# Kernel tuning notes

Hardware: AMD Instinct MI355X
Metric: run time of the kernel (lower is better)

The kernel has to match this reference:

```python
import jax, jax.numpy as jnp
import numpy as np

LAGS = 2
SLOPE = 0.01  # nn.LeakyReLU default negative_slope


def setup_inputs() -> dict:
    key = jax.random.key(0)
    k0, k1, k2, k3, k4 = jax.random.split(key, 5)
    B, T, D, H = 64, 514, 32, 128
    IN = LAGS * D + 1
    x = jax.random.normal(k0, (B, T, D), dtype=jnp.float32)
    # per-latent-dim 2-layer MLP params (num_layers=3, layer_norm=False collapses to 2 Linears)
    W1 = jax.random.normal(k1, (D, H, IN), dtype=jnp.float32) / np.sqrt(IN).astype(np.float32)
    b1 = jax.random.normal(k2, (D, H), dtype=jnp.float32) * 0.01
    W2 = jax.random.normal(k3, (D, H), dtype=jnp.float32) / np.sqrt(H).astype(np.float32)
    b2 = jax.random.normal(k4, (D,), dtype=jnp.float32) * 0.01
    return {"x": x, "W1": W1, "b1": b1, "W2": W2, "b2": b2}


def reference(x, W1, b1, W2, b2):
    L = LAGS
    B, T, D = x.shape
    # unfold(dim=1, size=L+1, step=1) + swapaxes -> windows [B, T-L, L+1, D]
    idx = jnp.arange(T - L)[:, None] + jnp.arange(L + 1)[None, :]
    w = x[:, idx]                       # [B, T-L, L+1, D]
    w = w.reshape(-1, L + 1, D)         # [N, L+1, D]
    yy = w[:, -1, :]                    # [N, D]  current step, per dim
    xx = w[:, :-1, :].reshape(-1, L * D)  # [N, L*D] lagged history (shared)
    # batched tiny-MLP forward: input to g_i is [xx, yy[:, i]]
    pre = (jnp.einsum('nk,dhk->ndh', xx, W1[:, :, :-1])
           + yy[:, :, None] * W1[:, :, -1][None]
           + b1[None])                  # [N, D, H]
    act = jnp.where(pre >= 0, pre, SLOPE * pre)
    residuals = jnp.einsum('ndh,dh->nd', act, W2) + b2[None]  # [N, D]
    # analytic Jacobian of scalar output wrt the (L*D+1)-dim input:
    # J = (W2 * leaky'(pre)) @ W1
    dact = jnp.where(pre >= 0, jnp.float32(1.0), jnp.float32(SLOPE))
    g = dact * W2[None]                 # [N, D, H]
    jac = jnp.einsum('ndh,dhk->ndk', g, W1)  # [N, D, L*D+1]
    logabsdet = jnp.sum(jnp.log(jnp.abs(jac[:, :, -1])), axis=1)  # [N] summed over dims
    # hist_jac: torch returns a list of D tensors [N, 1, L*D]; stacked here as [D, N, 1, L*D]
    hist_jac = jnp.transpose(jac[:, :, :-1], (1, 0, 2))[:, :, None, :]
    residuals = residuals.reshape(B, T - L, D)
    sum_log_abs_det_jacobian = logabsdet.reshape(B, T - L).sum(axis=1)  # [B]
    return residuals, sum_log_abs_det_jacobian, hist_jac
```

## Files before the change

kernel.cpp:

```cpp
#include <hip/hip_runtime.h>
#include <math.h>


typedef _Float16 f16;
typedef __attribute__((ext_vector_type(8))) _Float16 half8;
typedef __attribute__((ext_vector_type(4))) _Float16 half4;
typedef __attribute__((ext_vector_type(4))) float floatx4;

namespace {
constexpr int    XS_ROW   = 40;
constexpr size_t XS_SPLIT = (size_t)64 * 514 * XS_ROW * 2;
constexpr size_t WS_XS_HI = 0;
constexpr size_t WS_XS_LO = XS_SPLIT;
constexpr int    W1_KP    = 72;
constexpr size_t W1_SPLIT = (size_t)32 * 128 * W1_KP * 2;
constexpr size_t WS_W1_HI = 2 * XS_SPLIT;
constexpr size_t WS_W1_LO = WS_W1_HI + W1_SPLIT;
constexpr int    W1T_HP   = 136;
constexpr size_t WS_W1T   = WS_W1_LO + W1_SPLIT;

constexpr int L_W1HI = 0;
constexpr int L_W1LO = 18432;
constexpr int L_GB   = 0;
constexpr int L_W1T  = 17408;
constexpr int L_XSHI = 36864;
constexpr int L_XSLO = 42144;
constexpr int L_B1   = 47424;
constexpr int L_W2   = L_B1 + 512;
constexpr int L_W64  = L_W2 + 512;
constexpr int L_YY   = L_W64 + 512;
constexpr int L_RES  = L_YY + 256;
constexpr int L_JAC  = L_RES + 1024;
constexpr int L_TOTAL = L_JAC + 1024;

constexpr size_t OUT1_OFF = (size_t)64 * 512 * 32;
constexpr size_t OUT2_OFF = OUT1_OFF + 64;
}

__global__ __launch_bounds__(256) void split_x_kernel(
    const float* __restrict__ x, f16* __restrict__ xh, f16* __restrict__ xl)
{
    int idx = blockIdx.x * 256 + threadIdx.x;
    if (idx >= 64 * 514 * 32) return;
    int row = idx >> 5, c = idx & 31;
    float v = x[idx];
    f16 hi = (f16)v;
    float r = v - (float)hi;
    xh[row * XS_ROW + c] = hi;
    xl[row * XS_ROW + c] = (f16)(r * 4096.0f);
}

__global__ __launch_bounds__(256) void split_w1_kernel(
    const float* __restrict__ W1, f16* __restrict__ wh, f16* __restrict__ wl,
    f16* __restrict__ wT)
{
    int idx = blockIdx.x * 256 + threadIdx.x;
    if (idx >= 32 * 128 * 64) return;
    int d = idx >> 13, rem = idx & 8191;
    int h = rem >> 6, k = rem & 63;
    float v = W1[((size_t)(d * 128 + h)) * 65 + k];
    f16 hi = (f16)v;
    float r = v - (float)hi;
    wh[(size_t)(d * 128 + h) * W1_KP + k] = hi;
    wl[(size_t)(d * 128 + h) * W1_KP + k] = (f16)(r * 4096.0f);
    wT[(size_t)(d * 64 + k) * W1T_HP + h] = hi;
}

__global__ __launch_bounds__(256, 3) void np_main_kernel(
    const float* __restrict__ x,
    const float* __restrict__ W1,
    const float* __restrict__ b1,
    const float* __restrict__ W2,
    const float* __restrict__ b2,
    const char* __restrict__ ws,
    float* __restrict__ out)
{
    extern __shared__ char smem[];
    const int tile = blockIdx.x;
    const int d    = blockIdx.y;
    const int b    = tile >> 3;
    const int t0   = (tile & 7) << 6;
    const int tid  = threadIdx.x;
    const int wave = tid >> 6, lane = tid & 63;
    const int c = lane & 15, q = lane >> 4;

    float* b1L  = (float*)(smem + L_B1);
    float* W2L  = (float*)(smem + L_W2);
    float* w64L = (float*)(smem + L_W64);
    float* yyL  = (float*)(smem + L_YY);
    float* resP = (float*)(smem + L_RES);
    float* jacP = (float*)(smem + L_JAC);

    {
        const float4* s1 = (const float4*)(ws + WS_W1_HI + (size_t)d * 18432);
        const float4* s2 = (const float4*)(ws + WS_W1_LO + (size_t)d * 18432);
        float4* d1 = (float4*)(smem + L_W1HI);
        float4* d2 = (float4*)(smem + L_W1LO);
        for (int i = tid; i < 1152; i += 256) { d1[i] = s1[i]; d2[i] = s2[i]; }
        const float4* s3 = (const float4*)(ws + WS_XS_HI + (size_t)(b * 514 + t0) * (XS_ROW * 2));
        const float4* s4 = (const float4*)(ws + WS_XS_LO + (size_t)(b * 514 + t0) * (XS_ROW * 2));
        float4* d3 = (float4*)(smem + L_XSHI);
        float4* d4 = (float4*)(smem + L_XSLO);
        for (int i = tid; i < 330; i += 256) { d3[i] = s3[i]; d4[i] = s4[i]; }
        if (tid < 128) {
            b1L[tid]  = b1[d * 128 + tid];
            W2L[tid]  = W2[d * 128 + tid];
            w64L[tid] = W1[(size_t)(d * 128 + tid) * 65 + 64];
        }
        if (tid < 64) yyL[tid] = x[(size_t)(b * 514 + t0 + tid + 2) * 32 + d];
    }
    __syncthreads();

    floatx4 accP[2][4], accQ[2][4];
    #pragma unroll
    for (int ht = 0; ht < 2; ++ht)
        #pragma unroll
        for (int nt = 0; nt < 4; ++nt) { accP[ht][nt] = (floatx4)0.f; accQ[ht][nt] = (floatx4)0.f; }

    #pragma unroll
    for (int ks = 0; ks < 2; ++ks) {
        half8 aH[2], aL[2], bH[4], bL[4];
        #pragma unroll
        for (int ht = 0; ht < 2; ++ht) {
            const int off = (wave * 32 + ht * 16 + c) * W1_KP + ks * 32 + q * 8;
            aH[ht] = *(const half8*)(smem + L_W1HI + off * 2);
            aL[ht] = *(const half8*)(smem + L_W1LO + off * 2);
        }
        #pragma unroll
        for (int nt = 0; nt < 4; ++nt) {
            const int off = (nt * 16 + c + ks) * XS_ROW + q * 8;
            bH[nt] = *(const half8*)(smem + L_XSHI + off * 2);
            bL[nt] = *(const half8*)(smem + L_XSLO + off * 2);
        }
        #pragma unroll
        for (int ht = 0; ht < 2; ++ht)
            #pragma unroll
            for (int nt = 0; nt < 4; ++nt) {
                accP[ht][nt] = __builtin_amdgcn_mfma_f32_16x16x32_f16(aH[ht], bH[nt], accP[ht][nt], 0, 0, 0);
                accQ[ht][nt] = __builtin_amdgcn_mfma_f32_16x16x32_f16(aH[ht], bL[nt], accQ[ht][nt], 0, 0, 0);
                accQ[ht][nt] = __builtin_amdgcn_mfma_f32_16x16x32_f16(aL[ht], bH[nt], accQ[ht][nt], 0, 0, 0);
            }
    }
    __syncthreads();

    {
        const float4* s = (const float4*)(ws + WS_W1T + (size_t)d * 17408);
        float4* dst = (float4*)(smem + L_W1T);
        for (int i = tid; i < 1088; i += 256) dst[i] = s[i];
    }
    float res[4] = {0.f, 0.f, 0.f, 0.f}, j64[4] = {0.f, 0.f, 0.f, 0.f};
    #pragma unroll
    for (int ht = 0; ht < 2; ++ht) {
        const int hbase = wave * 32 + ht * 16 + q * 4;
        #pragma unroll
        for (int nt = 0; nt < 4; ++nt) {
            const int n = nt * 16 + c;
            half4 gp;
            #pragma unroll
            for (int r = 0; r < 4; ++r) {
                const int h = hbase + r;
                const float pre = accP[ht][nt][r] + accQ[ht][nt][r] * (1.0f / 4096.0f)
                                + b1L[h] + yyL[n] * w64L[h];
                const float gg = (pre >= 0.f ? 1.0f : 0.01f) * W2L[h];
                res[nt] += pre * gg;
                j64[nt] += gg * w64L[h];
                gp[r] = (f16)gg;
            }
            *(half4*)(smem + L_GB + (n * W1T_HP + hbase) * 2) = gp;
        }
    }
    #pragma unroll
    for (int nt = 0; nt < 4; ++nt) {
        float rv = res[nt];
        rv += __shfl_xor(rv, 16, 64);
        rv += __shfl_xor(rv, 32, 64);
        float jv = j64[nt];
        jv += __shfl_xor(jv, 16, 64);
        jv += __shfl_xor(jv, 32, 64);
        if (lane < 16) {
            resP[wave * 64 + nt * 16 + lane] = rv;
            jacP[wave * 64 + nt * 16 + lane] = jv;
        }
    }
    __syncthreads();

    if (tid < 64) {
        const int n = tid;
        float r = b2[d], j = 0.f;
        #pragma unroll
        for (int w = 0; w < 4; ++w) { r += resP[w * 64 + n]; j += jacP[w * 64 + n]; }
        out[(size_t)(b * 512 + t0 + n) * 32 + d] = r;
        float lg = logf(fabsf(j));
        #pragma unroll
        for (int off = 32; off > 0; off >>= 1) lg += __shfl_down(lg, off, 64);
        if (tid == 0) atomicAdd(out + OUT1_OFF + b, lg);
    }

    floatx4 acc2[4];
    #pragma unroll
    for (int kt = 0; kt < 4; ++kt) acc2[kt] = (floatx4)0.f;
    #pragma unroll
    for (int ks = 0; ks < 4; ++ks) {
        const half8 aF = *(const half8*)(smem + L_GB + ((wave * 16 + c) * W1T_HP + ks * 32 + q * 8) * 2);
        half8 bF[4];
        #pragma unroll
        for (int kt = 0; kt < 4; ++kt)
            bF[kt] = *(const half8*)(smem + L_W1T + ((kt * 16 + c) * W1T_HP + ks * 32 + q * 8) * 2);
        #pragma unroll
        for (int kt = 0; kt < 4; ++kt)
            acc2[kt] = __builtin_amdgcn_mfma_f32_16x16x32_f16(aF, bF[kt], acc2[kt], 0, 0, 0);
    }
    {
        float* out2 = out + OUT2_OFF + (size_t)d * ((size_t)32768 * 64)
                    + (size_t)(b * 512 + t0) * 64;
        #pragma unroll
        for (int kt = 0; kt < 4; ++kt)
            #pragma unroll
            for (int r = 0; r < 4; ++r)
                out2[(size_t)(wave * 16 + q * 4 + r) * 64 + kt * 16 + c] = acc2[kt][r];
    }
}

extern "C" void kernel_launch(void* const* d_in, const int* in_sizes, int n_in,
                              void* d_out, int out_size, void* d_ws, size_t ws_size,
                              hipStream_t stream) {
    const float* x  = (const float*)d_in[0];
    const float* W1 = (const float*)d_in[1];
    const float* b1 = (const float*)d_in[2];
    const float* W2 = (const float*)d_in[3];
    const float* b2 = (const float*)d_in[4];
    float* out = (float*)d_out;
    char* ws = (char*)d_ws;

    hipMemsetAsync(out + OUT1_OFF, 0, 64 * sizeof(float), stream);

    hipLaunchKernelGGL(split_x_kernel, dim3((64 * 514 * 32 + 255) / 256), dim3(256), 0, stream,
                       x, (f16*)(ws + WS_XS_HI), (f16*)(ws + WS_XS_LO));
    hipLaunchKernelGGL(split_w1_kernel, dim3((32 * 128 * 64 + 255) / 256), dim3(256), 0, stream,
                       W1, (f16*)(ws + WS_W1_HI), (f16*)(ws + WS_W1_LO), (f16*)(ws + WS_W1T));

    hipLaunchKernelGGL(np_main_kernel, dim3(512, 32), dim3(256), L_TOTAL, stream,
                       x, W1, b1, W2, b2, (const char*)ws, out);
}
```

Baseline: 415.2 us.

## Preswizzle W1 into MFMA fragment order, split x in-kernel, coalesce output stores

The x hi/lo split now happens inside the main kernel instead of a separate pass. W1 and its transpose are pre-laid-out in MFMA fragment order so the main kernel reads them straight from global memory rather than staging them through LDS. This drops a barrier and shrinks LDS enough to raise the occupancy target to 4 blocks per SM. The hist_jac output is transposed through LDS for coalesced float4 stores, and residuals are written in d-major order then transposed by a new small finishing kernel. The trade-off is more L2 traffic from repeated per-block weight fragment reads and one extra launch.

```diff
diff --git a/kernel.cpp b/kernel.cpp
--- a/kernel.cpp
+++ b/kernel.cpp
@@ -8,24 +8,20 @@
 typedef __attribute__((ext_vector_type(4))) float floatx4;
 
 namespace {
-constexpr int    XS_ROW   = 40;
-constexpr size_t XS_SPLIT = (size_t)64 * 514 * XS_ROW * 2;
-constexpr size_t WS_XS_HI = 0;
-constexpr size_t WS_XS_LO = XS_SPLIT;
-constexpr int    W1_KP    = 72;
-constexpr size_t W1_SPLIT = (size_t)32 * 128 * W1_KP * 2;
-constexpr size_t WS_W1_HI = 2 * XS_SPLIT;
-constexpr size_t WS_W1_LO = WS_W1_HI + W1_SPLIT;
-constexpr int    W1T_HP   = 136;
-constexpr size_t WS_W1T   = WS_W1_LO + W1_SPLIT;
-
-constexpr int L_W1HI = 0;
-constexpr int L_W1LO = 18432;
+constexpr size_t W1F_SZ    = (size_t)32 * 8192 * 2;
+constexpr size_t WS_W1F_HI = 0;
+constexpr size_t WS_W1F_LO = W1F_SZ;
+constexpr size_t WS_W1TF   = 2 * W1F_SZ;
+constexpr size_t WS_W64    = 3 * W1F_SZ;
+constexpr size_t WS_RES    = WS_W64 + (size_t)32 * 128 * 4;
+
+constexpr int XS_ROW = 40;
+constexpr int GB_HP  = 136;
+
 constexpr int L_GB   = 0;
-constexpr int L_W1T  = 17408;
-constexpr int L_XSHI = 36864;
-constexpr int L_XSLO = 42144;
-constexpr int L_B1   = 47424;
+constexpr int L_XSHI = 17408;
+constexpr int L_XSLO = L_XSHI + 5280;
+constexpr int L_B1   = L_XSLO + 5280;
 constexpr int L_W2   = L_B1 + 512;
 constexpr int L_W64  = L_W2 + 512;
 constexpr int L_YY   = L_W64 + 512;
@@ -37,22 +33,9 @@
 constexpr size_t OUT2_OFF = OUT1_OFF + 64;
 }
 
-__global__ __launch_bounds__(256) void split_x_kernel(
-    const float* __restrict__ x, f16* __restrict__ xh, f16* __restrict__ xl)
-{
-    int idx = blockIdx.x * 256 + threadIdx.x;
-    if (idx >= 64 * 514 * 32) return;
-    int row = idx >> 5, c = idx & 31;
-    float v = x[idx];
-    f16 hi = (f16)v;
-    float r = v - (float)hi;
-    xh[row * XS_ROW + c] = hi;
-    xl[row * XS_ROW + c] = (f16)(r * 4096.0f);
-}
-
 __global__ __launch_bounds__(256) void split_w1_kernel(
     const float* __restrict__ W1, f16* __restrict__ wh, f16* __restrict__ wl,
-    f16* __restrict__ wT)
+    f16* __restrict__ wT, float* __restrict__ w64)
 {
     int idx = blockIdx.x * 256 + threadIdx.x;
     if (idx >= 32 * 128 * 64) return;
@@ -61,18 +44,23 @@
     float v = W1[((size_t)(d * 128 + h)) * 65 + k];
     f16 hi = (f16)v;
     float r = v - (float)hi;
-    wh[(size_t)(d * 128 + h) * W1_KP + k] = hi;
-    wl[(size_t)(d * 128 + h) * W1_KP + k] = (f16)(r * 4096.0f);
-    wT[(size_t)(d * 64 + k) * W1T_HP + h] = hi;
-}
-
-__global__ __launch_bounds__(256, 3) void np_main_kernel(
+    int lane1 = (((k >> 3) & 3) << 4) | (h & 15);
+    size_t o1 = ((((size_t)d * 8 + (h >> 4)) * 2 + (k >> 5)) * 64 + lane1) * 8 + (k & 7);
+    wh[o1] = hi;
+    wl[o1] = (f16)(r * 4096.0f);
+    int lane2 = (((h >> 3) & 3) << 4) | (k & 15);
+    size_t o2 = ((((size_t)d * 4 + (h >> 5)) * 4 + (k >> 4)) * 64 + lane2) * 8 + (h & 7);
+    wT[o2] = hi;
+    if (k == 63) w64[d * 128 + h] = W1[((size_t)(d * 128 + h)) * 65 + 64];
+}
+
+__global__ __launch_bounds__(256, 4) void np_main_kernel(
     const float* __restrict__ x,
-    const float* __restrict__ W1,
     const float* __restrict__ b1,
     const float* __restrict__ W2,
     const float* __restrict__ b2,
     const char* __restrict__ ws,
+    float* __restrict__ resw,
     float* __restrict__ out)
 {
     extern __shared__ char smem[];
@@ -91,21 +79,31 @@
     float* resP = (float*)(smem + L_RES);
     float* jacP = (float*)(smem + L_JAC);
 
+    const f16* w1fh = (const f16*)(ws + WS_W1F_HI) + (size_t)d * 8192;
+    const f16* w1fl = (const f16*)(ws + WS_W1F_LO) + (size_t)d * 8192;
+    const f16* w1tf = (const f16*)(ws + WS_W1TF)   + (size_t)d * 8192;
+    const float* w64p = (const float*)(ws + WS_W64);
+
     {
-        const float4* s1 = (const float4*)(ws + WS_W1_HI + (size_t)d * 18432);
-        const float4* s2 = (const float4*)(ws + WS_W1_LO + (size_t)d * 18432);
-        float4* d1 = (float4*)(smem + L_W1HI);
-        float4* d2 = (float4*)(smem + L_W1LO);
-        for (int i = tid; i < 1152; i += 256) { d1[i] = s1[i]; d2[i] = s2[i]; }
-        const float4* s3 = (const float4*)(ws + WS_XS_HI + (size_t)(b * 514 + t0) * (XS_ROW * 2));
-        const float4* s4 = (const float4*)(ws + WS_XS_LO + (size_t)(b * 514 + t0) * (XS_ROW * 2));
-        float4* d3 = (float4*)(smem + L_XSHI);
-        float4* d4 = (float4*)(smem + L_XSLO);
-        for (int i = tid; i < 330; i += 256) { d3[i] = s3[i]; d4[i] = s4[i]; }
+        const float4* xs = (const float4*)(x + (size_t)(b * 514 + t0) * 32);
+        for (int u = tid; u < 528; u += 256) {
+            float4 v = xs[u];
+            int row = u >> 3, c4 = u & 7;
+            half4 hi, lo;
+            #pragma unroll
+            for (int j = 0; j < 4; ++j) {
+                float vv = (&v.x)[j];
+                f16 h = (f16)vv;
+                hi[j] = h;
+                lo[j] = (f16)((vv - (float)h) * 4096.0f);
+            }
+            *(half4*)(smem + L_XSHI + (row * XS_ROW + c4 * 4) * 2) = hi;
+            *(half4*)(smem + L_XSLO + (row * XS_ROW + c4 * 4) * 2) = lo;
+        }
         if (tid < 128) {
             b1L[tid]  = b1[d * 128 + tid];
             W2L[tid]  = W2[d * 128 + tid];
-            w64L[tid] = W1[(size_t)(d * 128 + tid) * 65 + 64];
+            w64L[tid] = w64p[d * 128 + tid];
         }
         if (tid < 64) yyL[tid] = x[(size_t)(b * 514 + t0 + tid + 2) * 32 + d];
     }
@@ -122,9 +120,9 @@
         half8 aH[2], aL[2], bH[4], bL[4];
         #pragma unroll
         for (int ht = 0; ht < 2; ++ht) {
-            const int off = (wave * 32 + ht * 16 + c) * W1_KP + ks * 32 + q * 8;
-            aH[ht] = *(const half8*)(smem + L_W1HI + off * 2);
-            aL[ht] = *(const half8*)(smem + L_W1LO + off * 2);
+            const int fo = (((wave * 2 + ht) * 2 + ks) * 64 + lane) * 8;
+            aH[ht] = *(const half8*)(w1fh + fo);
+            aL[ht] = *(const half8*)(w1fl + fo);
         }
         #pragma unroll
         for (int nt = 0; nt < 4; ++nt) {
@@ -141,13 +139,7 @@
                 accQ[ht][nt] = __builtin_amdgcn_mfma_f32_16x16x32_f16(aL[ht], bH[nt], accQ[ht][nt], 0, 0, 0);
             }
     }
-    __syncthreads();
-
-    {
-        const float4* s = (const float4*)(ws + WS_W1T + (size_t)d * 17408);
-        float4* dst = (float4*)(smem + L_W1T);
-        for (int i = tid; i < 1088; i += 256) dst[i] = s[i];
-    }
+
     float res[4] = {0.f, 0.f, 0.f, 0.f}, j64[4] = {0.f, 0.f, 0.f, 0.f};
     #pragma unroll
     for (int ht = 0; ht < 2; ++ht) {
@@ -166,7 +158,7 @@
                 j64[nt] += gg * w64L[h];
                 gp[r] = (f16)gg;
             }
-            *(half4*)(smem + L_GB + (n * W1T_HP + hbase) * 2) = gp;
+            *(half4*)(smem + L_GB + (n * GB_HP + hbase) * 2) = gp;
         }
     }
     #pragma unroll
@@ -189,7 +181,7 @@
         float r = b2[d], j = 0.f;
         #pragma unroll
         for (int w = 0; w < 4; ++w) { r += resP[w * 64 + n]; j += jacP[w * 64 + n]; }
-        out[(size_t)(b * 512 + t0 + n) * 32 + d] = r;
+        resw[(size_t)d * 32768 + (size_t)(b * 512 + t0) + n] = r;
         float lg = logf(fabsf(j));
         #pragma unroll
         for (int off = 32; off > 0; off >>= 1) lg += __shfl_down(lg, off, 64);
@@ -201,23 +193,51 @@
     for (int kt = 0; kt < 4; ++kt) acc2[kt] = (floatx4)0.f;
     #pragma unroll
     for (int ks = 0; ks < 4; ++ks) {
-        const half8 aF = *(const half8*)(smem + L_GB + ((wave * 16 + c) * W1T_HP + ks * 32 + q * 8) * 2);
+        const half8 aF = *(const half8*)(smem + L_GB + ((wave * 16 + c) * GB_HP + ks * 32 + q * 8) * 2);
         half8 bF[4];
         #pragma unroll
         for (int kt = 0; kt < 4; ++kt)
-            bF[kt] = *(const half8*)(smem + L_W1T + ((kt * 16 + c) * W1T_HP + ks * 32 + q * 8) * 2);
+            bF[kt] = *(const half8*)(w1tf + ((ks * 4 + kt) * 64 + lane) * 8);
         #pragma unroll
         for (int kt = 0; kt < 4; ++kt)
             acc2[kt] = __builtin_amdgcn_mfma_f32_16x16x32_f16(aF, bF[kt], acc2[kt], 0, 0, 0);
     }
+
     {
+        float* tp = (float*)(smem + L_GB + wave * (16 * GB_HP * 2));
+        #pragma unroll
+        for (int kt = 0; kt < 4; ++kt)
+            #pragma unroll
+            for (int r = 0; r < 4; ++r)
+                tp[(q * 4 + r) * 68 + kt * 16 + c] = acc2[kt][r];
         float* out2 = out + OUT2_OFF + (size_t)d * ((size_t)32768 * 64)
-                    + (size_t)(b * 512 + t0) * 64;
-        #pragma unroll
-        for (int kt = 0; kt < 4; ++kt)
-            #pragma unroll
-            for (int r = 0; r < 4; ++r)
-                out2[(size_t)(wave * 16 + q * 4 + r) * 64 + kt * 16 + c] = acc2[kt][r];
+                    + (size_t)(b * 512 + t0 + wave * 16) * 64;
+        #pragma unroll
+        for (int j = 0; j < 4; ++j) {
+            floatx4 v = *(const floatx4*)(tp + (j * 4 + q) * 68 + c * 4);
+            *(floatx4*)(out2 + (size_t)j * 256 + (size_t)lane * 4) = v;
+        }
+    }
+}
+
+__global__ __launch_bounds__(256) void finish_res_kernel(
+    const float* __restrict__ resw, float* __restrict__ out)
+{
+    __shared__ float tile[32][65];
+    const int n0 = blockIdx.x * 64;
+    const int tid = threadIdx.x;
+    #pragma unroll
+    for (int i = 0; i < 8; ++i) {
+        int idx = i * 256 + tid;
+        int dd = idx >> 6, n = idx & 63;
+        tile[dd][n] = resw[(size_t)dd * 32768 + n0 + n];
+    }
+    __syncthreads();
+    #pragma unroll
+    for (int i = 0; i < 8; ++i) {
+        int idx = i * 256 + tid;
+        int n = idx >> 5, dd = idx & 31;
+        out[(size_t)(n0 + n) * 32 + dd] = tile[dd][n];
     }
 }
 
@@ -234,11 +254,13 @@
 
     hipMemsetAsync(out + OUT1_OFF, 0, 64 * sizeof(float), stream);
 
-    hipLaunchKernelGGL(split_x_kernel, dim3((64 * 514 * 32 + 255) / 256), dim3(256), 0, stream,
-                       x, (f16*)(ws + WS_XS_HI), (f16*)(ws + WS_XS_LO));
     hipLaunchKernelGGL(split_w1_kernel, dim3((32 * 128 * 64 + 255) / 256), dim3(256), 0, stream,
-                       W1, (f16*)(ws + WS_W1_HI), (f16*)(ws + WS_W1_LO), (f16*)(ws + WS_W1T));
+                       W1, (f16*)(ws + WS_W1F_HI), (f16*)(ws + WS_W1F_LO),
+                       (f16*)(ws + WS_W1TF), (float*)(ws + WS_W64));
 
     hipLaunchKernelGGL(np_main_kernel, dim3(512, 32), dim3(256), L_TOTAL, stream,
-                       x, W1, b1, W2, b2, (const char*)ws, out);
-}
+                       x, b1, W2, b2, (const char*)ws, (float*)(ws + WS_RES), out);
+
+    hipLaunchKernelGGL(finish_res_kernel, dim3(512), dim3(256), 0, stream,
+                       (const float*)(ws + WS_RES), out);
+}
```

Measured after the change: 369.0 us. -11.1%, faster.
